# Kernel optimization log

Hardware: AMD Instinct MI355X
Metric: run time of the kernel (lower is better)

## Reference

```python
import jax, jax.numpy as jnp
import numpy as np

B = 4096
NUM_PTS = 1000

def de_boor(knotss, t, CP, p):
    # knotss: [N, K], t: [T, N], CP: [N, ncp, 2, 1] -> [T, N, 2, 1]
    N = knotss.shape[0]
    # k[b] = number of knots in knotss[b, p+1:] strictly below t (matches torch loop)
    k = jnp.sum((t[:, :, None] > knotss[None, :, p + 1:]).astype(jnp.int32), axis=-1)  # [T, N]
    bn = jnp.arange(N)[None, :, None]
    idx = k[:, :, None] + jnp.arange(p + 1)[None, None, :]           # [T, N, p+1]
    E = CP[bn, idx]                                                  # [T, N, p+1, 2, 1]
    te = t[:, :, None, None, None]
    for j in range(1, p + 1):
        m = p - j + 1
        i = jnp.arange(m)[None, None, :]
        a1 = knotss[bn, p + 1 + i + k[:, :, None]][..., None, None]  # [T, N, m, 1, 1]
        a2 = knotss[bn, i + j + k[:, :, None]][..., None, None]
        # in torch, ascending i reads old E[i+1]; vectorized update over old E is identical
        E = ((a1 - te) * E[:, :, :m] + (te - a2) * E[:, :, 1:m + 1]) / (a1 - a2)
    return E[:, :, 0]

def first_derivative(Pc, knots):
    n = Pc.shape[1]
    den = (knots[:, 4:n + 3] - knots[:, 1:n])[:, :, None, None]
    Q = 3.0 / den * (Pc[:, 1:] - Pc[:, :-1])
    return Q, knots[:, 1:-1]

def second_derivative(Q, knots):
    n = Q.shape[1]
    den = (knots[:, 3:n + 2] - knots[:, 1:n])[:, :, None, None]
    R = 2.0 / den * (Q[:, 1:] - Q[:, :-1])
    return R, knots[:, 1:-1]

def construct(t, knots, p=3):
    # t: [B], knots: [B, K] -> N: [B, K-1]; replicates stale-tail behavior of torch loop
    K = knots.shape[1]
    N = ((t[:, None] >= knots[:, :-1]) & (t[:, None] < knots[:, 1:])).astype(knots.dtype)
    lenN = K - 2
    for power in range(1, p + 1):
        m = lenN - power
        den_a = knots[:, power:power + m] - knots[:, :m]
        a = jnp.where(den_a != 0, (t[:, None] - knots[:, :m]) / jnp.where(den_a != 0, den_a, 1.0), 0.0)
        den_b = knots[:, power + 1:power + 1 + m] - knots[:, 1:1 + m]
        b = jnp.where(den_b != 0, (knots[:, power + 1:power + 1 + m] - t[:, None]) / jnp.where(den_b != 0, den_b, 1.0), 0.0)
        N = N.at[:, :m].set(N[:, :m] * a + N[:, 1:m + 1] * b)
    return N

def construct_A(knots):
    # knots: [B, 12], 6 data points -> A: [B, 8, 8]
    Bn = knots.shape[0]
    rows = [construct(knots[:, i + 3], knots) for i in range(5)]
    # i == 5 hits the knots[0, 8] == 1 branch (clamped right end): one-hot at column 7
    row5 = jnp.zeros((Bn, knots.shape[1] - 1), knots.dtype).at[:, 7].set(1.0)
    A = jnp.stack(rows + [row5], axis=1)[:, :, :8]                   # [B, 6, 8]
    z = jnp.zeros((Bn, 1, 8), knots.dtype)
    A = jnp.concatenate([z, A, z], axis=1)                           # [B, 8, 8]
    A = A.at[:, 0, 0].add(knots[:, 5]).at[:, 0, 1].add(-knots[:, 4] - knots[:, 5]).at[:, 0, 2].add(knots[:, 4])
    A = A.at[:, -1, -3].add(1.0 - knots[:, 7]).at[:, -1, -2].add(knots[:, 7] + knots[:, 6] - 2.0).at[:, -1, -1].add(1.0 - knots[:, 6])
    return A

def solve(P, knots):
    Bn = P.shape[0]
    z = jnp.zeros((Bn, 1, 1), P.dtype)
    Px = jnp.concatenate([z, P[:, :, 0], z], axis=1)  # [B, 8, 1]
    Py = jnp.concatenate([z, P[:, :, 1], z], axis=1)
    inv = jnp.linalg.inv(construct_A(knots))
    Cx = inv @ Px
    Cy = inv @ Py
    return jnp.concatenate([Cx, Cy], axis=2)[..., None]  # [B, 8, 2, 1]

def forward(x, P, W1, b1, W2, b2, W3, b3):
    h = jax.nn.relu(x @ W1.T + b1)
    h = jax.nn.relu(h @ W2.T + b2)
    xs = jax.nn.softmax(h @ W3.T + b3, axis=1)  # [B, 5]
    # torch: w[:, i] = x[:, i] + detach(w[:, i-1]) -> cumsum in value, identity in grad
    x4 = xs[:, :4]
    w = x4 + jax.lax.stop_gradient(jnp.cumsum(x4, axis=1) - x4)
    Bn = x.shape[0]
    knots = jnp.concatenate([jnp.zeros((Bn, 4), x.dtype), w, jnp.ones((Bn, 4), x.dtype)], axis=1)  # [B, 12]
    C = solve(P, knots)  # [B, 8, 2, 1]
    # global curvature over linspace(knots[0,3]=0, knots[0,10]=1, NUM_PTS)
    L = jnp.linspace(0.0, 1.0, NUM_PTS).astype(x.dtype)
    tall = jnp.broadcast_to(L[:, None], (NUM_PTS, Bn))
    Q, dk = first_derivative(C, knots)
    R, ddk = second_derivative(Q, dk)
    sp = de_boor(dk, tall, Q, 2)    # [T, B, 2, 1] spline'
    sdp = de_boor(ddk, tall, R, 1)  # [T, B, 2, 1] spline''
    spx, spy = sp[:, :, 0, 0], sp[:, :, 1, 0]
    sdx, sdy = sdp[:, :, 0, 0], sdp[:, :, 1, 0]
    speed2 = spx ** 2 + spy ** 2
    curv = (spx * sdy - spy * sdx) / (speed2 ** 3) ** 0.5
    vals = curv ** 2 * jnp.sqrt(speed2)  # [T, B]; de_boor(knots2, J, Q, 2) == spline', reused
    S1 = vals[1::2].sum(axis=0)
    S2 = vals[0::2].sum(axis=0)
    h_step = 1.0 / (NUM_PTS - 1)
    integration = h_step / 3.0 * (4.0 * S1 + 2.0 * S2)
    return integration, knots

def setup_inputs():
    key = jax.random.key(0)
    ks = jax.random.split(key, 8)
    return {
        "x": jax.random.normal(ks[0], (B, 8), jnp.float32),
        "P": jax.random.normal(ks[1], (B, 6, 2, 1), jnp.float32),
        "W1": jax.random.normal(ks[2], (128, 8), jnp.float32) * 0.3,
        "b1": jnp.full((128,), 0.01, jnp.float32),
        "W2": jax.random.normal(ks[3], (128, 128), jnp.float32) * 0.09,
        "b2": jnp.full((128,), 0.01, jnp.float32),
        "W3": jax.random.normal(ks[4], (5, 128), jnp.float32) * 0.1,
        "b3": jnp.full((5,), 0.01, jnp.float32),
    }

def reference(x, P, W1, b1, W2, b2, W3, b3):
    return forward(x, P, W1, b1, W2, b2, W3, b3)
```

## Files before the change

### kernel.cpp

```cpp
#include <hip/hip_runtime.h>
#include <math.h>

#define BATCH 4096
#define NPTS 1000

#define WSYNC() do { asm volatile("s_waitcnt lgkmcnt(0)" ::: "memory"); \
                     __builtin_amdgcn_sched_barrier(0); } while (0)

__device__ __forceinline__ float frcp(float v) { return __builtin_amdgcn_rcpf(v); }

__global__ __launch_bounds__(256) void k12_mlp_prep(
    const float* __restrict__ x, const float* __restrict__ P,
    const float* __restrict__ W1, const float* __restrict__ b1,
    const float* __restrict__ W2, const float* __restrict__ b2,
    const float* __restrict__ W3, const float* __restrict__ b3,
    float* __restrict__ coef, float* __restrict__ out_knots)
{
    __shared__ float s_h1[8][128];
    __shared__ float s_part[4][4][5];
    __shared__ float LA[8][8][10];
    __shared__ float LQ[8][16];
    __shared__ float LR[8][16];

    const int tid = threadIdx.x;
    const int wv = tid >> 6, lane = tid & 63;
    const int p = tid >> 7, row = tid & 127;
    const int b0 = blockIdx.x * 8;

    {
        float4 w0 = ((const float4*)(W1 + row * 8))[0];
        float4 w1 = ((const float4*)(W1 + row * 8))[1];
        float bb = b1[row];
        #pragma unroll
        for (int k = 0; k < 4; ++k) {
            const float* xr = x + (b0 + p * 4 + k) * 8;
            float4 xa = ((const float4*)xr)[0];
            float4 xb = ((const float4*)xr)[1];
            float h = bb + w0.x*xa.x + w0.y*xa.y + w0.z*xa.z + w0.w*xa.w
                         + w1.x*xb.x + w1.y*xb.y + w1.z*xb.z + w1.w*xb.w;
            s_h1[p * 4 + k][row] = fmaxf(h, 0.f);
        }
    }
    __syncthreads();

    float bb2 = b2[row];
    float a0 = bb2, a1 = bb2, a2 = bb2, a3 = bb2;
    {
        const float4* wr = (const float4*)(W2 + row * 128);
        const float4* h0 = (const float4*)s_h1[p * 4 + 0];
        const float4* h1 = (const float4*)s_h1[p * 4 + 1];
        const float4* h2p = (const float4*)s_h1[p * 4 + 2];
        const float4* h3 = (const float4*)s_h1[p * 4 + 3];
        #pragma unroll 8
        for (int c4 = 0; c4 < 32; ++c4) {
            float4 w = wr[c4];
            float4 ha = h0[c4], hb = h1[c4], hc = h2p[c4], hd = h3[c4];
            a0 += w.x*ha.x + w.y*ha.y + w.z*ha.z + w.w*ha.w;
            a1 += w.x*hb.x + w.y*hb.y + w.z*hb.z + w.w*hb.w;
            a2 += w.x*hc.x + w.y*hc.y + w.z*hc.z + w.w*hc.w;
            a3 += w.x*hd.x + w.y*hd.y + w.z*hd.z + w.w*hd.w;
        }
    }
    float h2_0 = fmaxf(a0, 0.f), h2_1 = fmaxf(a1, 0.f);
    float h2_2 = fmaxf(a2, 0.f), h2_3 = fmaxf(a3, 0.f);

    #pragma unroll
    for (int c = 0; c < 5; ++c) {
        float wc = W3[c * 128 + row];
        float p0 = wc * h2_0, p1 = wc * h2_1, p2 = wc * h2_2, p3 = wc * h2_3;
        #pragma unroll
        for (int m = 32; m >= 1; m >>= 1) {
            p0 += __shfl_xor(p0, m, 64);
            p1 += __shfl_xor(p1, m, 64);
            p2 += __shfl_xor(p2, m, 64);
            p3 += __shfl_xor(p3, m, 64);
        }
        if (lane == 0) {
            s_part[wv][0][c] = p0; s_part[wv][1][c] = p1;
            s_part[wv][2][c] = p2; s_part[wv][3][c] = p3;
        }
    }
    __syncthreads();
    if (wv != 0) return;

    const int el = lane >> 3, r = lane & 7;
    const int e = b0 + el;
    const int pw = (el >> 2) * 2;

    float lg0 = s_part[pw][el & 3][0] + s_part[pw + 1][el & 3][0] + b3[0];
    float lg1 = s_part[pw][el & 3][1] + s_part[pw + 1][el & 3][1] + b3[1];
    float lg2 = s_part[pw][el & 3][2] + s_part[pw + 1][el & 3][2] + b3[2];
    float lg3 = s_part[pw][el & 3][3] + s_part[pw + 1][el & 3][3] + b3[3];
    float lg4 = s_part[pw][el & 3][4] + s_part[pw + 1][el & 3][4] + b3[4];
    float mx = fmaxf(fmaxf(fmaxf(fmaxf(lg0, lg1), lg2), lg3), lg4);
    float e0 = expf(lg0-mx), e1 = expf(lg1-mx), e2 = expf(lg2-mx),
          e3 = expf(lg3-mx), e4 = expf(lg4-mx);
    float s = e0 + e1 + e2 + e3 + e4;
    float xs0 = e0/s, xs1 = e1/s, xs2 = e2/s, xs3 = e3/s;
    float c0 = xs0, c1 = c0 + xs1, c2 = c1 + xs2, c3 = c2 + xs3;
    float w4 = xs0 + (c0 - xs0);
    float w5 = xs1 + (c1 - xs1);
    float w6 = xs2 + (c2 - xs2);
    float w7 = xs3 + (c3 - xs3);

    {
        float kv = (r < 4) ? 0.f : (r == 4 ? w4 : r == 5 ? w5 : r == 6 ? w6 : w7);
        out_knots[e * 12 + r] = kv;
        if (r < 4) {
            out_knots[e * 12 + 8 + r] = 1.f;
            coef[e * 64 + 60 + r] = (r == 0 ? w4 : r == 1 ? w5 : r == 2 ? w6 : w7);
        }
    }

    const float ka[12] = {0.f,0.f,0.f,0.f,w4,w5,w6,w7,1.f,1.f,1.f,1.f};
    float t = (r == 2) ? w4 : (r == 3) ? w5 : (r == 4) ? w6 : (r == 5) ? w7 : 0.f;
    float N[11];
    #pragma unroll
    for (int i = 0; i < 11; ++i)
        N[i] = (t >= ka[i] && t < ka[i+1]) ? 1.f : 0.f;
    #pragma unroll
    for (int pq = 1; pq <= 3; ++pq) {
        #pragma unroll
        for (int i = 0; i < 10; ++i) {
            if (i < 10 - pq) {
                float da = ka[i+pq] - ka[i];
                float av = (da != 0.f) ? (t - ka[i]) * frcp(da) : 0.f;
                float db = ka[i+pq+1] - ka[i+1];
                float bv = (db != 0.f) ? (ka[i+pq+1] - t) * frcp(db) : 0.f;
                N[i] = N[i] * av + N[i+1] * bv;
            }
        }
    }

    float a[10];
    #pragma unroll
    for (int c = 0; c < 8; ++c) {
        float v0 = (c==0) ? w5 : (c==1) ? (-w4-w5) : (c==2) ? w4 : 0.f;
        float v6 = (c==7) ? 1.f : 0.f;
        float v7 = (c==5) ? (1.f-w7) : (c==6) ? (w7+w6-2.f) : (c==7) ? (1.f-w6) : 0.f;
        float vb = (r==0) ? v0 : (r==6) ? v6 : v7;
        a[c] = (r >= 1 && r <= 5) ? N[c] : vb;
    }
    {
        float px = 0.f, py = 0.f;
        if (r >= 1 && r <= 6) {
            px = P[e * 12 + (r-1) * 2 + 0];
            py = P[e * 12 + (r-1) * 2 + 1];
        }
        a[8] = px; a[9] = py;
    }

    int done = 0, pcol = 7;
    #pragma unroll
    for (int col = 0; col < 8; ++col) {
        float bv = done ? -1.f : fabsf(a[col]);
        int bi = lane;
        #pragma unroll
        for (int m = 1; m <= 4; m <<= 1) {
            float ov = __shfl_xor(bv, m, 64);
            int   oi = __shfl_xor(bi, m, 64);
            if (ov > bv || (ov == bv && oi < bi)) { bv = ov; bi = oi; }
        }
        float pr[10];
        #pragma unroll
        for (int c = 0; c < 10; ++c) pr[c] = __shfl(a[c], bi, 64);
        if (lane == bi) { done = 1; pcol = col; }
        else if (!done) {
            float f = a[col] * frcp(pr[col]);
            #pragma unroll
            for (int c = 0; c < 10; ++c) if (c > col) a[c] -= f * pr[c];
        }
    }
    #pragma unroll
    for (int c = 0; c < 10; ++c) LA[el][pcol][c] = a[c];
    WSYNC();

    if (r < 2) {
        const int par = r;
        float C[8];
        #pragma unroll
        for (int col = 7; col >= 0; --col) {
            float sv = LA[el][col][8 + par];
            #pragma unroll
            for (int c = col + 1; c < 8; ++c) sv -= LA[el][col][c] * C[c];
            C[col] = sv * frcp(LA[el][col][col]);
        }
        float Qr[7], Rr[6];
        const float dq[7] = { w4, w5, w6, w7 - w4, 1.f - w5, 1.f - w6, 1.f - w7 };
        #pragma unroll
        for (int i = 0; i < 7; ++i) Qr[i] = (3.f * frcp(dq[i])) * (C[i+1] - C[i]);
        const float dr[6] = { w4, w5, w6 - w4, w7 - w5, 1.f - w6, 1.f - w7 };
        #pragma unroll
        for (int i = 0; i < 6; ++i) Rr[i] = (2.f * frcp(dr[i])) * (Qr[i+1] - Qr[i]);
        #pragma unroll
        for (int i = 0; i < 7; ++i) LQ[el][i*2+par] = Qr[i];
        #pragma unroll
        for (int i = 0; i < 6; ++i) LR[el][i*2+par] = Rr[i];
    }
    WSYNC();

    if (r < 5) {
        const int s5 = r;
        float k2 = (s5 <= 1) ? 0.f : (s5 == 2) ? w4 : (s5 == 3) ? w5 : w6;
        float k3 = (s5 == 0) ? 0.f : (s5 == 1) ? w4 : (s5 == 2) ? w5 : (s5 == 3) ? w6 : w7;
        float k4 = (s5 == 0) ? w4 : (s5 == 1) ? w5 : (s5 == 2) ? w6 : (s5 == 3) ? w7 : 1.f;
        float k5 = (s5 == 0) ? w5 : (s5 == 1) ? w6 : (s5 == 2) ? w7 : 1.f;
        float q0x = LQ[el][s5*2],     q0y = LQ[el][s5*2+1];
        float q1x = LQ[el][(s5+1)*2], q1y = LQ[el][(s5+1)*2+1];
        float q2x = LQ[el][(s5+2)*2], q2y = LQ[el][(s5+2)*2+1];
        float r0x = LR[el][s5*2],     r0y = LR[el][s5*2+1];
        float r1x = LR[el][(s5+1)*2], r1y = LR[el][(s5+1)*2+1];
        float r42 = frcp(k4-k2), r53 = frcp(k5-k3), r43 = frcp(k4-k3);
        float A0x = (k4*q0x - k2*q1x)*r42, B0x = (q1x-q0x)*r42;
        float A1x = (k5*q1x - k3*q2x)*r53, B1x = (q2x-q1x)*r53;
        float c0x = r43*(k4*A0x - k3*A1x);
        float c1x = r43*(k4*B0x - A0x + A1x - k3*B1x);
        float c2x = r43*(B1x - B0x);
        float e0x = r43*(k4*r0x - k3*r1x);
        float e1x = r43*(r1x - r0x);
        float A0y = (k4*q0y - k2*q1y)*r42, B0y = (q1y-q0y)*r42;
        float A1y = (k5*q1y - k3*q2y)*r53, B1y = (q2y-q1y)*r53;
        float c0y = r43*(k4*A0y - k3*A1y);
        float c1y = r43*(k4*B0y - A0y + A1y - k3*B1y);
        float c2y = r43*(B1y - B0y);
        float e0y = r43*(k4*r0y - k3*r1y);
        float e1y = r43*(r1y - r0y);
        float* cb = coef + e * 64 + s5 * 12;
        cb[0] = c0x; cb[1] = c1x; cb[2]  = c2x; cb[3]  = c0y;
        cb[4] = c1y; cb[5] = c2y; cb[6]  = e0x; cb[7]  = e1x;
        cb[8] = e0y; cb[9] = e1y; cb[10] = 0.f; cb[11] = 0.f;
    }
}

__global__ __launch_bounds__(256) void k3_eval(
    const float* __restrict__ coef, float* __restrict__ out_integ)
{
    const int tid = threadIdx.x, wv = tid >> 6, lane = tid & 63;
    const int e = blockIdx.x * 4 + wv;
    const float c999 = 1.f / 999.f;

    float v = coef[e * 64 + lane];
    int vi = __float_as_int(v);
    float w4 = __int_as_float(__builtin_amdgcn_readlane(vi, 60));
    float w5 = __int_as_float(__builtin_amdgcn_readlane(vi, 61));
    float w6 = __int_as_float(__builtin_amdgcn_readlane(vi, 62));
    float w7 = __int_as_float(__builtin_amdgcn_readlane(vi, 63));

    auto bsearch = [&](float w) {
        int lo = 0, hi = 1000;
        #pragma unroll
        for (int it = 0; it < 10; ++it) {
            int mid = (lo + hi) >> 1;
            bool pr = ((float)mid * c999 > w);
            hi = pr ? mid : hi;
            lo = pr ? lo : (mid + 1);
        }
        return lo;
    };
    int B0 = bsearch(w4), B1 = bsearch(w5), B2 = bsearch(w6), B3 = bsearch(w7);

    float acc = 0.f;
    #define DOSEG(S, LOE, HIE) { \
        float cx0 = __int_as_float(__builtin_amdgcn_readlane(vi, (S)*12+0)); \
        float cx1 = __int_as_float(__builtin_amdgcn_readlane(vi, (S)*12+1)); \
        float cx2 = __int_as_float(__builtin_amdgcn_readlane(vi, (S)*12+2)); \
        float cy0 = __int_as_float(__builtin_amdgcn_readlane(vi, (S)*12+3)); \
        float cy1 = __int_as_float(__builtin_amdgcn_readlane(vi, (S)*12+4)); \
        float cy2 = __int_as_float(__builtin_amdgcn_readlane(vi, (S)*12+5)); \
        float ex0 = __int_as_float(__builtin_amdgcn_readlane(vi, (S)*12+6)); \
        float ex1 = __int_as_float(__builtin_amdgcn_readlane(vi, (S)*12+7)); \
        float ey0 = __int_as_float(__builtin_amdgcn_readlane(vi, (S)*12+8)); \
        float ey1 = __int_as_float(__builtin_amdgcn_readlane(vi, (S)*12+9)); \
        int lo = (LOE), hi = (HIE); \
        float wl = ((lo + lane) & 1) ? 4.f : 2.f; \
        for (int idx = lo + lane; idx < hi; idx += 64) { \
            float tt = (float)idx * c999; \
            float spx = (cx2 * tt + cx1) * tt + cx0; \
            float spy = (cy2 * tt + cy1) * tt + cy0; \
            float sdx = ex1 * tt + ex0; \
            float sdy = ey1 * tt + ey0; \
            float s2 = spx * spx + spy * spy; \
            float cross = spx * sdy - spy * sdx; \
            float rs = rsqrtf(s2); \
            float rs2 = rs * rs; \
            acc += wl * (cross * cross * (rs2 * rs2 * rs)); \
        } }
    DOSEG(0, 0,  B0)
    DOSEG(1, B0, B1)
    DOSEG(2, B1, B2)
    DOSEG(3, B2, B3)
    DOSEG(4, B3, 1000)
    #undef DOSEG

    #pragma unroll
    for (int m = 32; m >= 1; m >>= 1) acc += __shfl_xor(acc, m, 64);
    if (lane == 0) out_integ[e] = (1.f / 999.f) / 3.f * acc;
}

extern "C" void kernel_launch(void* const* d_in, const int* in_sizes, int n_in,
                              void* d_out, int out_size, void* d_ws, size_t ws_size,
                              hipStream_t stream) {
    const float* x  = (const float*)d_in[0];
    const float* P  = (const float*)d_in[1];
    const float* W1 = (const float*)d_in[2];
    const float* b1 = (const float*)d_in[3];
    const float* W2 = (const float*)d_in[4];
    const float* b2 = (const float*)d_in[5];
    const float* W3 = (const float*)d_in[6];
    const float* b3 = (const float*)d_in[7];
    float* out_integ = (float*)d_out;
    float* out_knots = out_integ + BATCH;

    float* coefb = (float*)d_ws;

    k12_mlp_prep<<<dim3(BATCH / 8), dim3(256), 0, stream>>>(
        x, P, W1, b1, W2, b2, W3, b3, coefb, out_knots);
    k3_eval<<<dim3(BATCH / 4), dim3(256), 0, stream>>>(coefb, out_integ);
}
```

Measured before the change: 29.95 us.

## Fuse MLP/spline-prep and curvature-eval kernels into one via shared-memory coefficients

Merges the two kernels into a single launch. Per-element spline coefficients are kept in LDS instead of round-tripping through a global workspace, and each of the 4 waves then evaluates 2 elements' curvature integrals after a block barrier. This removes one kernel launch and the global write/read of coefficients. In exchange, the serial solve done only by wave 0 now blocks the other waves before evaluation, there are 512 blocks instead of 1024, and the launch-bounds occupancy hint is raised.

After: 28.84 us. 1.04x faster.

```diff
diff --git a/kernel.cpp b/kernel.cpp
--- a/kernel.cpp
+++ b/kernel.cpp
@@ -9,18 +9,19 @@
 
 __device__ __forceinline__ float frcp(float v) { return __builtin_amdgcn_rcpf(v); }
 
-__global__ __launch_bounds__(256) void k12_mlp_prep(
+__global__ __launch_bounds__(256, 8) void net2_one(
     const float* __restrict__ x, const float* __restrict__ P,
     const float* __restrict__ W1, const float* __restrict__ b1,
     const float* __restrict__ W2, const float* __restrict__ b2,
     const float* __restrict__ W3, const float* __restrict__ b3,
-    float* __restrict__ coef, float* __restrict__ out_knots)
+    float* __restrict__ out_integ, float* __restrict__ out_knots)
 {
     __shared__ float s_h1[8][128];
     __shared__ float s_part[4][4][5];
     __shared__ float LA[8][8][10];
     __shared__ float LQ[8][16];
     __shared__ float LR[8][16];
+    __shared__ float s_coef[8][64];
 
     const int tid = threadIdx.x;
     const int wv = tid >> 6, lane = tid & 63;
@@ -81,220 +82,220 @@
         }
     }
     __syncthreads();
-    if (wv != 0) return;
-
-    const int el = lane >> 3, r = lane & 7;
-    const int e = b0 + el;
-    const int pw = (el >> 2) * 2;
-
-    float lg0 = s_part[pw][el & 3][0] + s_part[pw + 1][el & 3][0] + b3[0];
-    float lg1 = s_part[pw][el & 3][1] + s_part[pw + 1][el & 3][1] + b3[1];
-    float lg2 = s_part[pw][el & 3][2] + s_part[pw + 1][el & 3][2] + b3[2];
-    float lg3 = s_part[pw][el & 3][3] + s_part[pw + 1][el & 3][3] + b3[3];
-    float lg4 = s_part[pw][el & 3][4] + s_part[pw + 1][el & 3][4] + b3[4];
-    float mx = fmaxf(fmaxf(fmaxf(fmaxf(lg0, lg1), lg2), lg3), lg4);
-    float e0 = expf(lg0-mx), e1 = expf(lg1-mx), e2 = expf(lg2-mx),
-          e3 = expf(lg3-mx), e4 = expf(lg4-mx);
-    float s = e0 + e1 + e2 + e3 + e4;
-    float xs0 = e0/s, xs1 = e1/s, xs2 = e2/s, xs3 = e3/s;
-    float c0 = xs0, c1 = c0 + xs1, c2 = c1 + xs2, c3 = c2 + xs3;
-    float w4 = xs0 + (c0 - xs0);
-    float w5 = xs1 + (c1 - xs1);
-    float w6 = xs2 + (c2 - xs2);
-    float w7 = xs3 + (c3 - xs3);
-
-    {
-        float kv = (r < 4) ? 0.f : (r == 4 ? w4 : r == 5 ? w5 : r == 6 ? w6 : w7);
-        out_knots[e * 12 + r] = kv;
-        if (r < 4) {
-            out_knots[e * 12 + 8 + r] = 1.f;
-            coef[e * 64 + 60 + r] = (r == 0 ? w4 : r == 1 ? w5 : r == 2 ? w6 : w7);
-        }
-    }
-
-    const float ka[12] = {0.f,0.f,0.f,0.f,w4,w5,w6,w7,1.f,1.f,1.f,1.f};
-    float t = (r == 2) ? w4 : (r == 3) ? w5 : (r == 4) ? w6 : (r == 5) ? w7 : 0.f;
-    float N[11];
+
+    if (wv == 0) {
+        const int el = lane >> 3, r = lane & 7;
+        const int e = b0 + el;
+        const int pw = (el >> 2) * 2;
+
+        float lg0 = s_part[pw][el & 3][0] + s_part[pw + 1][el & 3][0] + b3[0];
+        float lg1 = s_part[pw][el & 3][1] + s_part[pw + 1][el & 3][1] + b3[1];
+        float lg2 = s_part[pw][el & 3][2] + s_part[pw + 1][el & 3][2] + b3[2];
+        float lg3 = s_part[pw][el & 3][3] + s_part[pw + 1][el & 3][3] + b3[3];
+        float lg4 = s_part[pw][el & 3][4] + s_part[pw + 1][el & 3][4] + b3[4];
+        float mx = fmaxf(fmaxf(fmaxf(fmaxf(lg0, lg1), lg2), lg3), lg4);
+        float e0 = expf(lg0-mx), e1 = expf(lg1-mx), e2 = expf(lg2-mx),
+              e3 = expf(lg3-mx), e4 = expf(lg4-mx);
+        float s = e0 + e1 + e2 + e3 + e4;
+        float xs0 = e0/s, xs1 = e1/s, xs2 = e2/s, xs3 = e3/s;
+        float c0 = xs0, c1 = c0 + xs1, c2 = c1 + xs2, c3 = c2 + xs3;
+        float w4 = xs0 + (c0 - xs0);
+        float w5 = xs1 + (c1 - xs1);
+        float w6 = xs2 + (c2 - xs2);
+        float w7 = xs3 + (c3 - xs3);
+
+        {
+            float kv = (r < 4) ? 0.f : (r == 4 ? w4 : r == 5 ? w5 : r == 6 ? w6 : w7);
+            out_knots[e * 12 + r] = kv;
+            if (r < 4) {
+                out_knots[e * 12 + 8 + r] = 1.f;
+                s_coef[el][60 + r] = (r == 0 ? w4 : r == 1 ? w5 : r == 2 ? w6 : w7);
+            }
+        }
+
+        const float ka[12] = {0.f,0.f,0.f,0.f,w4,w5,w6,w7,1.f,1.f,1.f,1.f};
+        float t = (r == 2) ? w4 : (r == 3) ? w5 : (r == 4) ? w6 : (r == 5) ? w7 : 0.f;
+        float N[11];
+        #pragma unroll
+        for (int i = 0; i < 11; ++i)
+            N[i] = (t >= ka[i] && t < ka[i+1]) ? 1.f : 0.f;
+        #pragma unroll
+        for (int pq = 1; pq <= 3; ++pq) {
+            #pragma unroll
+            for (int i = 0; i < 10; ++i) {
+                if (i < 10 - pq) {
+                    float da = ka[i+pq] - ka[i];
+                    float av = (da != 0.f) ? (t - ka[i]) * frcp(da) : 0.f;
+                    float db = ka[i+pq+1] - ka[i+1];
+                    float bv = (db != 0.f) ? (ka[i+pq+1] - t) * frcp(db) : 0.f;
+                    N[i] = N[i] * av + N[i+1] * bv;
+                }
+            }
+        }
+
+        float a[10];
+        #pragma unroll
+        for (int c = 0; c < 8; ++c) {
+            float v0 = (c==0) ? w5 : (c==1) ? (-w4-w5) : (c==2) ? w4 : 0.f;
+            float v6 = (c==7) ? 1.f : 0.f;
+            float v7 = (c==5) ? (1.f-w7) : (c==6) ? (w7+w6-2.f) : (c==7) ? (1.f-w6) : 0.f;
+            float vb = (r==0) ? v0 : (r==6) ? v6 : v7;
+            a[c] = (r >= 1 && r <= 5) ? N[c] : vb;
+        }
+        {
+            float px = 0.f, py = 0.f;
+            if (r >= 1 && r <= 6) {
+                px = P[e * 12 + (r-1) * 2 + 0];
+                py = P[e * 12 + (r-1) * 2 + 1];
+            }
+            a[8] = px; a[9] = py;
+        }
+
+        int done = 0, pcol = 7;
+        #pragma unroll
+        for (int col = 0; col < 8; ++col) {
+            float bv = done ? -1.f : fabsf(a[col]);
+            int bi = lane;
+            #pragma unroll
+            for (int m = 1; m <= 4; m <<= 1) {
+                float ov = __shfl_xor(bv, m, 64);
+                int   oi = __shfl_xor(bi, m, 64);
+                if (ov > bv || (ov == bv && oi < bi)) { bv = ov; bi = oi; }
+            }
+            float pr[10];
+            #pragma unroll
+            for (int c = 0; c < 10; ++c) pr[c] = __shfl(a[c], bi, 64);
+            if (lane == bi) { done = 1; pcol = col; }
+            else if (!done) {
+                float f = a[col] * frcp(pr[col]);
+                #pragma unroll
+                for (int c = 0; c < 10; ++c) if (c > col) a[c] -= f * pr[c];
+            }
+        }
+        #pragma unroll
+        for (int c = 0; c < 10; ++c) LA[el][pcol][c] = a[c];
+        WSYNC();
+
+        if (r < 2) {
+            const int par = r;
+            float C[8];
+            #pragma unroll
+            for (int col = 7; col >= 0; --col) {
+                float sv = LA[el][col][8 + par];
+                #pragma unroll
+                for (int c = col + 1; c < 8; ++c) sv -= LA[el][col][c] * C[c];
+                C[col] = sv * frcp(LA[el][col][col]);
+            }
+            float Qr[7], Rr[6];
+            const float dq[7] = { w4, w5, w6, w7 - w4, 1.f - w5, 1.f - w6, 1.f - w7 };
+            #pragma unroll
+            for (int i = 0; i < 7; ++i) Qr[i] = (3.f * frcp(dq[i])) * (C[i+1] - C[i]);
+            const float dr[6] = { w4, w5, w6 - w4, w7 - w5, 1.f - w6, 1.f - w7 };
+            #pragma unroll
+            for (int i = 0; i < 6; ++i) Rr[i] = (2.f * frcp(dr[i])) * (Qr[i+1] - Qr[i]);
+            #pragma unroll
+            for (int i = 0; i < 7; ++i) LQ[el][i*2+par] = Qr[i];
+            #pragma unroll
+            for (int i = 0; i < 6; ++i) LR[el][i*2+par] = Rr[i];
+        }
+        WSYNC();
+
+        if (r < 5) {
+            const int s5 = r;
+            float k2 = (s5 <= 1) ? 0.f : (s5 == 2) ? w4 : (s5 == 3) ? w5 : w6;
+            float k3 = (s5 == 0) ? 0.f : (s5 == 1) ? w4 : (s5 == 2) ? w5 : (s5 == 3) ? w6 : w7;
+            float k4 = (s5 == 0) ? w4 : (s5 == 1) ? w5 : (s5 == 2) ? w6 : (s5 == 3) ? w7 : 1.f;
+            float k5 = (s5 == 0) ? w5 : (s5 == 1) ? w6 : (s5 == 2) ? w7 : 1.f;
+            float q0x = LQ[el][s5*2],     q0y = LQ[el][s5*2+1];
+            float q1x = LQ[el][(s5+1)*2], q1y = LQ[el][(s5+1)*2+1];
+            float q2x = LQ[el][(s5+2)*2], q2y = LQ[el][(s5+2)*2+1];
+            float r0x = LR[el][s5*2],     r0y = LR[el][s5*2+1];
+            float r1x = LR[el][(s5+1)*2], r1y = LR[el][(s5+1)*2+1];
+            float r42 = frcp(k4-k2), r53 = frcp(k5-k3), r43 = frcp(k4-k3);
+            float A0x = (k4*q0x - k2*q1x)*r42, B0x = (q1x-q0x)*r42;
+            float A1x = (k5*q1x - k3*q2x)*r53, B1x = (q2x-q1x)*r53;
+            float c0x = r43*(k4*A0x - k3*A1x);
+            float c1x = r43*(k4*B0x - A0x + A1x - k3*B1x);
+            float c2x = r43*(B1x - B0x);
+            float e0x = r43*(k4*r0x - k3*r1x);
+            float e1x = r43*(r1x - r0x);
+            float A0y = (k4*q0y - k2*q1y)*r42, B0y = (q1y-q0y)*r42;
+            float A1y = (k5*q1y - k3*q2y)*r53, B1y = (q2y-q1y)*r53;
+            float c0y = r43*(k4*A0y - k3*A1y);
+            float c1y = r43*(k4*B0y - A0y + A1y - k3*B1y);
+            float c2y = r43*(B1y - B0y);
+            float e0y = r43*(k4*r0y - k3*r1y);
+            float e1y = r43*(r1y - r0y);
+            float* cb = &s_coef[el][s5 * 12];
+            cb[0] = c0x; cb[1] = c1x; cb[2]  = c2x; cb[3]  = c0y;
+            cb[4] = c1y; cb[5] = c2y; cb[6]  = e0x; cb[7]  = e1x;
+            cb[8] = e0y; cb[9] = e1y; cb[10] = 0.f; cb[11] = 0.f;
+        }
+    }
+    __syncthreads();
+
+    const float c999 = 1.f / 999.f;
     #pragma unroll
-    for (int i = 0; i < 11; ++i)
-        N[i] = (t >= ka[i] && t < ka[i+1]) ? 1.f : 0.f;
-    #pragma unroll
-    for (int pq = 1; pq <= 3; ++pq) {
-        #pragma unroll
-        for (int i = 0; i < 10; ++i) {
-            if (i < 10 - pq) {
-                float da = ka[i+pq] - ka[i];
-                float av = (da != 0.f) ? (t - ka[i]) * frcp(da) : 0.f;
-                float db = ka[i+pq+1] - ka[i+1];
-                float bv = (db != 0.f) ? (ka[i+pq+1] - t) * frcp(db) : 0.f;
-                N[i] = N[i] * av + N[i+1] * bv;
-            }
-        }
-    }
-
-    float a[10];
-    #pragma unroll
-    for (int c = 0; c < 8; ++c) {
-        float v0 = (c==0) ? w5 : (c==1) ? (-w4-w5) : (c==2) ? w4 : 0.f;
-        float v6 = (c==7) ? 1.f : 0.f;
-        float v7 = (c==5) ? (1.f-w7) : (c==6) ? (w7+w6-2.f) : (c==7) ? (1.f-w6) : 0.f;
-        float vb = (r==0) ? v0 : (r==6) ? v6 : v7;
-        a[c] = (r >= 1 && r <= 5) ? N[c] : vb;
-    }
-    {
-        float px = 0.f, py = 0.f;
-        if (r >= 1 && r <= 6) {
-            px = P[e * 12 + (r-1) * 2 + 0];
-            py = P[e * 12 + (r-1) * 2 + 1];
-        }
-        a[8] = px; a[9] = py;
-    }
-
-    int done = 0, pcol = 7;
-    #pragma unroll
-    for (int col = 0; col < 8; ++col) {
-        float bv = done ? -1.f : fabsf(a[col]);
-        int bi = lane;
-        #pragma unroll
-        for (int m = 1; m <= 4; m <<= 1) {
-            float ov = __shfl_xor(bv, m, 64);
-            int   oi = __shfl_xor(bi, m, 64);
-            if (ov > bv || (ov == bv && oi < bi)) { bv = ov; bi = oi; }
-        }
-        float pr[10];
-        #pragma unroll
-        for (int c = 0; c < 10; ++c) pr[c] = __shfl(a[c], bi, 64);
-        if (lane == bi) { done = 1; pcol = col; }
-        else if (!done) {
-            float f = a[col] * frcp(pr[col]);
-            #pragma unroll
-            for (int c = 0; c < 10; ++c) if (c > col) a[c] -= f * pr[c];
-        }
-    }
-    #pragma unroll
-    for (int c = 0; c < 10; ++c) LA[el][pcol][c] = a[c];
-    WSYNC();
-
-    if (r < 2) {
-        const int par = r;
-        float C[8];
-        #pragma unroll
-        for (int col = 7; col >= 0; --col) {
-            float sv = LA[el][col][8 + par];
-            #pragma unroll
-            for (int c = col + 1; c < 8; ++c) sv -= LA[el][col][c] * C[c];
-            C[col] = sv * frcp(LA[el][col][col]);
-        }
-        float Qr[7], Rr[6];
-        const float dq[7] = { w4, w5, w6, w7 - w4, 1.f - w5, 1.f - w6, 1.f - w7 };
-        #pragma unroll
-        for (int i = 0; i < 7; ++i) Qr[i] = (3.f * frcp(dq[i])) * (C[i+1] - C[i]);
-        const float dr[6] = { w4, w5, w6 - w4, w7 - w5, 1.f - w6, 1.f - w7 };
-        #pragma unroll
-        for (int i = 0; i < 6; ++i) Rr[i] = (2.f * frcp(dr[i])) * (Qr[i+1] - Qr[i]);
-        #pragma unroll
-        for (int i = 0; i < 7; ++i) LQ[el][i*2+par] = Qr[i];
-        #pragma unroll
-        for (int i = 0; i < 6; ++i) LR[el][i*2+par] = Rr[i];
-    }
-    WSYNC();
-
-    if (r < 5) {
-        const int s5 = r;
-        float k2 = (s5 <= 1) ? 0.f : (s5 == 2) ? w4 : (s5 == 3) ? w5 : w6;
-        float k3 = (s5 == 0) ? 0.f : (s5 == 1) ? w4 : (s5 == 2) ? w5 : (s5 == 3) ? w6 : w7;
-        float k4 = (s5 == 0) ? w4 : (s5 == 1) ? w5 : (s5 == 2) ? w6 : (s5 == 3) ? w7 : 1.f;
-        float k5 = (s5 == 0) ? w5 : (s5 == 1) ? w6 : (s5 == 2) ? w7 : 1.f;
-        float q0x = LQ[el][s5*2],     q0y = LQ[el][s5*2+1];
-        float q1x = LQ[el][(s5+1)*2], q1y = LQ[el][(s5+1)*2+1];
-        float q2x = LQ[el][(s5+2)*2], q2y = LQ[el][(s5+2)*2+1];
-        float r0x = LR[el][s5*2],     r0y = LR[el][s5*2+1];
-        float r1x = LR[el][(s5+1)*2], r1y = LR[el][(s5+1)*2+1];
-        float r42 = frcp(k4-k2), r53 = frcp(k5-k3), r43 = frcp(k4-k3);
-        float A0x = (k4*q0x - k2*q1x)*r42, B0x = (q1x-q0x)*r42;
-        float A1x = (k5*q1x - k3*q2x)*r53, B1x = (q2x-q1x)*r53;
-        float c0x = r43*(k4*A0x - k3*A1x);
-        float c1x = r43*(k4*B0x - A0x + A1x - k3*B1x);
-        float c2x = r43*(B1x - B0x);
-        float e0x = r43*(k4*r0x - k3*r1x);
-        float e1x = r43*(r1x - r0x);
-        float A0y = (k4*q0y - k2*q1y)*r42, B0y = (q1y-q0y)*r42;
-        float A1y = (k5*q1y - k3*q2y)*r53, B1y = (q2y-q1y)*r53;
-        float c0y = r43*(k4*A0y - k3*A1y);
-        float c1y = r43*(k4*B0y - A0y + A1y - k3*B1y);
-        float c2y = r43*(B1y - B0y);
-        float e0y = r43*(k4*r0y - k3*r1y);
-        float e1y = r43*(r1y - r0y);
-        float* cb = coef + e * 64 + s5 * 12;
-        cb[0] = c0x; cb[1] = c1x; cb[2]  = c2x; cb[3]  = c0y;
-        cb[4] = c1y; cb[5] = c2y; cb[6]  = e0x; cb[7]  = e1x;
-        cb[8] = e0y; cb[9] = e1y; cb[10] = 0.f; cb[11] = 0.f;
-    }
-}
-
-__global__ __launch_bounds__(256) void k3_eval(
-    const float* __restrict__ coef, float* __restrict__ out_integ)
-{
-    const int tid = threadIdx.x, wv = tid >> 6, lane = tid & 63;
-    const int e = blockIdx.x * 4 + wv;
-    const float c999 = 1.f / 999.f;
-
-    float v = coef[e * 64 + lane];
-    int vi = __float_as_int(v);
-    float w4 = __int_as_float(__builtin_amdgcn_readlane(vi, 60));
-    float w5 = __int_as_float(__builtin_amdgcn_readlane(vi, 61));
-    float w6 = __int_as_float(__builtin_amdgcn_readlane(vi, 62));
-    float w7 = __int_as_float(__builtin_amdgcn_readlane(vi, 63));
-
-    auto bsearch = [&](float w) {
-        int lo = 0, hi = 1000;
-        #pragma unroll
-        for (int it = 0; it < 10; ++it) {
-            int mid = (lo + hi) >> 1;
-            bool pr = ((float)mid * c999 > w);
-            hi = pr ? mid : hi;
-            lo = pr ? lo : (mid + 1);
-        }
-        return lo;
-    };
-    int B0 = bsearch(w4), B1 = bsearch(w5), B2 = bsearch(w6), B3 = bsearch(w7);
-
-    float acc = 0.f;
-    #define DOSEG(S, LOE, HIE) { \
-        float cx0 = __int_as_float(__builtin_amdgcn_readlane(vi, (S)*12+0)); \
-        float cx1 = __int_as_float(__builtin_amdgcn_readlane(vi, (S)*12+1)); \
-        float cx2 = __int_as_float(__builtin_amdgcn_readlane(vi, (S)*12+2)); \
-        float cy0 = __int_as_float(__builtin_amdgcn_readlane(vi, (S)*12+3)); \
-        float cy1 = __int_as_float(__builtin_amdgcn_readlane(vi, (S)*12+4)); \
-        float cy2 = __int_as_float(__builtin_amdgcn_readlane(vi, (S)*12+5)); \
-        float ex0 = __int_as_float(__builtin_amdgcn_readlane(vi, (S)*12+6)); \
-        float ex1 = __int_as_float(__builtin_amdgcn_readlane(vi, (S)*12+7)); \
-        float ey0 = __int_as_float(__builtin_amdgcn_readlane(vi, (S)*12+8)); \
-        float ey1 = __int_as_float(__builtin_amdgcn_readlane(vi, (S)*12+9)); \
-        int lo = (LOE), hi = (HIE); \
-        float wl = ((lo + lane) & 1) ? 4.f : 2.f; \
-        for (int idx = lo + lane; idx < hi; idx += 64) { \
-            float tt = (float)idx * c999; \
-            float spx = (cx2 * tt + cx1) * tt + cx0; \
-            float spy = (cy2 * tt + cy1) * tt + cy0; \
-            float sdx = ex1 * tt + ex0; \
-            float sdy = ey1 * tt + ey0; \
-            float s2 = spx * spx + spy * spy; \
-            float cross = spx * sdy - spy * sdx; \
-            float rs = rsqrtf(s2); \
-            float rs2 = rs * rs; \
-            acc += wl * (cross * cross * (rs2 * rs2 * rs)); \
-        } }
-    DOSEG(0, 0,  B0)
-    DOSEG(1, B0, B1)
-    DOSEG(2, B1, B2)
-    DOSEG(3, B2, B3)
-    DOSEG(4, B3, 1000)
-    #undef DOSEG
-
-    #pragma unroll
-    for (int m = 32; m >= 1; m >>= 1) acc += __shfl_xor(acc, m, 64);
-    if (lane == 0) out_integ[e] = (1.f / 999.f) / 3.f * acc;
+    for (int q = 0; q < 2; ++q) {
+        const int el = wv * 2 + q;
+        const int e = b0 + el;
+        float v = s_coef[el][lane];
+        int vi = __float_as_int(v);
+        float w4 = __int_as_float(__builtin_amdgcn_readlane(vi, 60));
+        float w5 = __int_as_float(__builtin_amdgcn_readlane(vi, 61));
+        float w6 = __int_as_float(__builtin_amdgcn_readlane(vi, 62));
+        float w7 = __int_as_float(__builtin_amdgcn_readlane(vi, 63));
+
+        auto bsearch = [&](float w) {
+            int lo = 0, hi = 1000;
+            #pragma unroll
+            for (int it = 0; it < 10; ++it) {
+                int mid = (lo + hi) >> 1;
+                bool pr = ((float)mid * c999 > w);
+                hi = pr ? mid : hi;
+                lo = pr ? lo : (mid + 1);
+            }
+            return lo;
+        };
+        int B0 = bsearch(w4), B1 = bsearch(w5), B2 = bsearch(w6), B3 = bsearch(w7);
+
+        float acc = 0.f;
+        #define DOSEG(S, LOE, HIE) { \
+            float cx0 = __int_as_float(__builtin_amdgcn_readlane(vi, (S)*12+0)); \
+            float cx1 = __int_as_float(__builtin_amdgcn_readlane(vi, (S)*12+1)); \
+            float cx2 = __int_as_float(__builtin_amdgcn_readlane(vi, (S)*12+2)); \
+            float cy0 = __int_as_float(__builtin_amdgcn_readlane(vi, (S)*12+3)); \
+            float cy1 = __int_as_float(__builtin_amdgcn_readlane(vi, (S)*12+4)); \
+            float cy2 = __int_as_float(__builtin_amdgcn_readlane(vi, (S)*12+5)); \
+            float ex0 = __int_as_float(__builtin_amdgcn_readlane(vi, (S)*12+6)); \
+            float ex1 = __int_as_float(__builtin_amdgcn_readlane(vi, (S)*12+7)); \
+            float ey0 = __int_as_float(__builtin_amdgcn_readlane(vi, (S)*12+8)); \
+            float ey1 = __int_as_float(__builtin_amdgcn_readlane(vi, (S)*12+9)); \
+            int lo = (LOE), hi = (HIE); \
+            float wl = ((lo + lane) & 1) ? 4.f : 2.f; \
+            for (int idx = lo + lane; idx < hi; idx += 64) { \
+                float tt = (float)idx * c999; \
+                float spx = (cx2 * tt + cx1) * tt + cx0; \
+                float spy = (cy2 * tt + cy1) * tt + cy0; \
+                float sdx = ex1 * tt + ex0; \
+                float sdy = ey1 * tt + ey0; \
+                float s2 = spx * spx + spy * spy; \
+                float cross = spx * sdy - spy * sdx; \
+                float rs = rsqrtf(s2); \
+                float rs2 = rs * rs; \
+                acc += wl * (cross * cross * (rs2 * rs2 * rs)); \
+            } }
+        DOSEG(0, 0,  B0)
+        DOSEG(1, B0, B1)
+        DOSEG(2, B1, B2)
+        DOSEG(3, B2, B3)
+        DOSEG(4, B3, 1000)
+        #undef DOSEG
+
+        #pragma unroll
+        for (int m = 32; m >= 1; m >>= 1) acc += __shfl_xor(acc, m, 64);
+        if (lane == 0) out_integ[e] = (1.f / 999.f) / 3.f * acc;
+    }
 }
 
 extern "C" void kernel_launch(void* const* d_in, const int* in_sizes, int n_in,
@@ -311,9 +312,6 @@
     float* out_integ = (float*)d_out;
     float* out_knots = out_integ + BATCH;
 
-    float* coefb = (float*)d_ws;
-
-    k12_mlp_prep<<<dim3(BATCH / 8), dim3(256), 0, stream>>>(
-        x, P, W1, b1, W2, b2, W3, b3, coefb, out_knots);
-    k3_eval<<<dim3(BATCH / 4), dim3(256), 0, stream>>>(coefb, out_integ);
+    net2_one<<<dim3(BATCH / 8), dim3(256), 0, stream>>>(
+        x, P, W1, b1, W2, b2, W3, b3, out_integ, out_knots);
 }
```
